# Optimization experiments

Hardware: AMD Instinct MI355X
Metric: run time of the kernel (lower is better)

The kernel has to match this reference:

```python
import jax, jax.numpy as jnp
import numpy as np
from math import sqrt

SCALE = sqrt(512.0)  # max(key_size, attn_hidden_size, query_size) with scaled=True

def setup_inputs() -> dict:
    key = jax.random.key(0)
    k1, k2, k3, k4, k5 = jax.random.split(key, 5)
    B, T, S, M, N, H = 8, 512, 512, 512, 512, 128
    return {
        "query": jax.random.normal(k1, (B, T, M), dtype=jnp.float32),
        "keys": jax.random.normal(k2, (B, S, N), dtype=jnp.float32),
        "W1": jax.random.normal(k3, (N, H), dtype=jnp.float32),
        "W2": jax.random.normal(k4, (M, H), dtype=jnp.float32),
        "v": jax.random.normal(k5, (H,), dtype=jnp.float32),
    }

def reference(query, keys, W1, W2, v):
    # Project query and keys into attention hidden space
    x1 = jnp.einsum('btm,mh->bth', query, W2)   # (B,T,H)
    x2 = jnp.einsum('bsn,nh->bsh', keys, W1)    # (B,S,H)
    # Broadcast merge (op='add'), tanh activation, v-weighted reduction over H
    merged = jnp.tanh(x1[:, :, None, :] + x2[:, None, :, :])  # (B,T,S,H)
    score = jnp.einsum('btsh,h->bts', merged, v)
    return score / SCALE
```

## Files before the change

kernel.cpp:

```cpp
#include <hip/hip_runtime.h>


constexpr float SCALE_IN  = 2.8853900817779268f;
constexpr float INV_SCALE = 0.04419417382415922f;

__global__ __launch_bounds__(512) void proj_kernel(
    const float* __restrict__ q,  const float* __restrict__ w2,
    const float* __restrict__ kk, const float* __restrict__ w1,
    float* __restrict__ x1w, float* __restrict__ x2w) {
  int blk = blockIdx.x;
  const float* A; const float* W; float* O;
  if (blk < 128) { A = q;  W = w2; O = x1w; }
  else           { blk -= 128; A = kk; W = w1; O = x2w; }

  const int tid = threadIdx.x;
  const int h   = tid & 127;
  const int rg  = tid >> 7;
  const int rbase = __builtin_amdgcn_readfirstlane(blk * 32 + rg * 8);

  float acc[8];
#pragma unroll
  for (int r = 0; r < 8; ++r) acc[r] = 0.0f;

  for (int m = 0; m < 512; m += 4) {
    const float wa = W[(m + 0) * 128 + h];
    const float wb = W[(m + 1) * 128 + h];
    const float wc = W[(m + 2) * 128 + h];
    const float wd = W[(m + 3) * 128 + h];
#pragma unroll
    for (int r = 0; r < 8; ++r) {
      const float4 a = *(const float4*)(A + (rbase + r) * 512 + m);
      acc[r] = fmaf(a.x, wa, acc[r]);
      acc[r] = fmaf(a.y, wb, acc[r]);
      acc[r] = fmaf(a.z, wc, acc[r]);
      acc[r] = fmaf(a.w, wd, acc[r]);
    }
  }
#pragma unroll
  for (int r = 0; r < 8; ++r)
    O[(rbase + r) * 128 + h] = acc[r] * SCALE_IN;
}

__global__ __launch_bounds__(256) void score_kernel(
    const float* __restrict__ x1w, const float* __restrict__ x2w,
    const float* __restrict__ v, float* __restrict__ out) {
  __shared__ float x1l[128 * 64];
  __shared__ float x2l[128 * 64];
  __shared__ float vl[128];

  const int tid   = threadIdx.x;
  const int b     = blockIdx.x >> 6;
  const int tile  = blockIdx.x & 63;
  const int tbase = (tile >> 3) * 64;
  const int sbase = (tile & 7) * 64;

  const float4* x1g = (const float4*)(x1w + (b * 512 + tbase) * 128);
  const float4* x2g = (const float4*)(x2w + (b * 512 + sbase) * 128);

  if (tid < 32) ((float4*)vl)[tid] = ((const float4*)v)[tid];

  const int l  = tid & 63;
  const int wv = tid >> 6;
#pragma unroll
  for (int p = 0; p < 8; ++p) {
    const int row = (l & 31) + 32 * (p & 1);
    const int c4  = (l >> 5) + 2 * wv + 8 * (p >> 1);
    const float4 a = x1g[row * 32 + c4];
    x1l[(4 * c4 + 0) * 64 + row] = a.x;
    x1l[(4 * c4 + 1) * 64 + row] = a.y;
    x1l[(4 * c4 + 2) * 64 + row] = a.z;
    x1l[(4 * c4 + 3) * 64 + row] = a.w;
    const float4 c = x2g[row * 32 + c4];
    x2l[(4 * c4 + 0) * 64 + row] = c.x;
    x2l[(4 * c4 + 1) * 64 + row] = c.y;
    x2l[(4 * c4 + 2) * 64 + row] = c.z;
    x2l[(4 * c4 + 3) * 64 + row] = c.w;
  }
  __syncthreads();

  const int sg = tid & 15;
  const int tg = tid >> 4;

  float racc[16];
#pragma unroll
  for (int i = 0; i < 16; ++i) racc[i] = 0.0f;
  float sv = 0.0f;

#pragma unroll 4
  for (int h = 0; h < 128; ++h) {
    const float4 tf = *(const float4*)(x1l + h * 64 + 4 * tg);
    const float4 sf = *(const float4*)(x2l + h * 64 + 4 * sg);
    const float vh = vl[h];
    sv += vh;
    const float ts[4] = {tf.x, tf.y, tf.z, tf.w};
    const float ss[4] = {sf.x, sf.y, sf.z, sf.w};
#pragma unroll
    for (int i = 0; i < 4; ++i) {
#pragma unroll
      for (int j = 0; j < 4; ++j) {
        const float e = __builtin_amdgcn_exp2f(ts[i] + ss[j]);
        const float r = __builtin_amdgcn_rcpf(e + 1.0f);
        racc[i * 4 + j] = fmaf(vh, r, racc[i * 4 + j]);
      }
    }
  }

  const float c1 = sv * INV_SCALE;
  const float c2 = -2.0f * INV_SCALE;
#pragma unroll
  for (int i = 0; i < 4; ++i) {
    const int t = tbase + 4 * tg + i;
    float4 o;
    o.x = fmaf(racc[i * 4 + 0], c2, c1);
    o.y = fmaf(racc[i * 4 + 1], c2, c1);
    o.z = fmaf(racc[i * 4 + 2], c2, c1);
    o.w = fmaf(racc[i * 4 + 3], c2, c1);
    *(float4*)(out + (size_t)(b * 512 + t) * 512 + sbase + 4 * sg) = o;
  }
}

extern "C" void kernel_launch(void* const* d_in, const int* in_sizes, int n_in,
                              void* d_out, int out_size, void* d_ws, size_t ws_size,
                              hipStream_t stream) {
  const float* query = (const float*)d_in[0];
  const float* keys  = (const float*)d_in[1];
  const float* W1    = (const float*)d_in[2];
  const float* W2    = (const float*)d_in[3];
  const float* v     = (const float*)d_in[4];
  float* out = (float*)d_out;

  float* x1w = (float*)d_ws;
  float* x2w = x1w + 8 * 512 * 128;

  hipLaunchKernelGGL(proj_kernel, dim3(256), dim3(512), 0, stream,
                     query, W2, keys, W1, x1w, x2w);
  hipLaunchKernelGGL(score_kernel, dim3(512), dim3(256), 0, stream,
                     x1w, x2w, v, out);
}
```

Before: 170.3 us.

## Precompute exp factors in projection and batch four reciprocals per rcp in score

The projection kernel now stores each exp2 value factored as an integer exponent plus an fp16 mantissa, packed into 32 bits. The score kernel rebuilds exp(x1+x2) with a multiply and ldexp instead of calling exp2 per element. It also sums four v-weighted reciprocals over a common denominator, so one rcp serves four h values. The projection GEMM moves to LDS tiling, and the score kernel runs 512 threads with fewer outputs per thread. This cuts transcendental work in the hot loop, but fp16 mantissas and the exponent clamp lose precision, and multiplying four terms into one denominator risks overflow.

```diff
diff --git a/kernel.cpp b/kernel.cpp
--- a/kernel.cpp
+++ b/kernel.cpp
@@ -1,4 +1,5 @@
 #include <hip/hip_runtime.h>
+#include <hip/hip_fp16.h>
 
 
 constexpr float SCALE_IN  = 2.8853900817779268f;
@@ -6,47 +7,81 @@
 
 __global__ __launch_bounds__(512) void proj_kernel(
     const float* __restrict__ q,  const float* __restrict__ w2,
-    const float* __restrict__ kk, const float* __restrict__ w1,
-    float* __restrict__ x1w, float* __restrict__ x2w) {
+    const float* __restrict__ ky, const float* __restrict__ w1,
+    unsigned int* __restrict__ x1w, unsigned int* __restrict__ x2w) {
+  __shared__ float As[32 * 64];
+  __shared__ float Ws[64 * 128];
+
   int blk = blockIdx.x;
-  const float* A; const float* W; float* O;
+  const float* A; const float* W; unsigned int* O;
   if (blk < 128) { A = q;  W = w2; O = x1w; }
-  else           { blk -= 128; A = kk; W = w1; O = x2w; }
-
+  else           { blk -= 128; A = ky; W = w1; O = x2w; }
+  const int rbase = blk * 32;
   const int tid = threadIdx.x;
-  const int h   = tid & 127;
-  const int rg  = tid >> 7;
-  const int rbase = __builtin_amdgcn_readfirstlane(blk * 32 + rg * 8);
-
-  float acc[8];
-#pragma unroll
-  for (int r = 0; r < 8; ++r) acc[r] = 0.0f;
-
-  for (int m = 0; m < 512; m += 4) {
-    const float wa = W[(m + 0) * 128 + h];
-    const float wb = W[(m + 1) * 128 + h];
-    const float wc = W[(m + 2) * 128 + h];
-    const float wd = W[(m + 3) * 128 + h];
-#pragma unroll
-    for (int r = 0; r < 8; ++r) {
-      const float4 a = *(const float4*)(A + (rbase + r) * 512 + m);
-      acc[r] = fmaf(a.x, wa, acc[r]);
-      acc[r] = fmaf(a.y, wb, acc[r]);
-      acc[r] = fmaf(a.z, wc, acc[r]);
-      acc[r] = fmaf(a.w, wd, acc[r]);
-    }
-  }
-#pragma unroll
-  for (int r = 0; r < 8; ++r)
-    O[(rbase + r) * 128 + h] = acc[r] * SCALE_IN;
+
+  const int rq = tid >> 5;
+  const int hq = tid & 31;
+
+  float acc[2][4];
+#pragma unroll
+  for (int r = 0; r < 2; ++r)
+#pragma unroll
+    for (int c = 0; c < 4; ++c) acc[r][c] = 0.0f;
+
+  for (int kb = 0; kb < 512; kb += 64) {
+    {
+      const int arow = tid >> 4;
+      const int kq4  = (tid & 15) * 4;
+      *(float4*)(As + arow * 64 + kq4) =
+          *(const float4*)(A + (size_t)(rbase + arow) * 512 + kb + kq4);
+      const int wrow = tid >> 5;
+      const int hq4  = (tid & 31) * 4;
+#pragma unroll
+      for (int p = 0; p < 4; ++p)
+        *(float4*)(Ws + (wrow + 16 * p) * 128 + hq4) =
+            *(const float4*)(W + (size_t)(kb + wrow + 16 * p) * 128 + hq4);
+    }
+    __syncthreads();
+#pragma unroll 4
+    for (int k4 = 0; k4 < 64; k4 += 4) {
+      float a[2][4], w[4][4];
+      *(float4*)a[0] = *(const float4*)(As + (2 * rq + 0) * 64 + k4);
+      *(float4*)a[1] = *(const float4*)(As + (2 * rq + 1) * 64 + k4);
+#pragma unroll
+      for (int kk = 0; kk < 4; ++kk)
+        *(float4*)w[kk] = *(const float4*)(Ws + (k4 + kk) * 128 + 4 * hq);
+#pragma unroll
+      for (int kk = 0; kk < 4; ++kk)
+#pragma unroll
+        for (int r = 0; r < 2; ++r)
+#pragma unroll
+          for (int c = 0; c < 4; ++c)
+            acc[r][c] = fmaf(a[r][kk], w[kk][c], acc[r][c]);
+    }
+    __syncthreads();
+  }
+
+#pragma unroll
+  for (int r = 0; r < 2; ++r) {
+    unsigned int pk[4];
+#pragma unroll
+    for (int c = 0; c < 4; ++c) {
+      const float z  = acc[r][c] * SCALE_IN;
+      const float kf = rintf(z);
+      const int   ki = (int)kf;
+      const float em = __builtin_amdgcn_exp2f(z - kf);
+      const __half hh = __float2half_rn(em);
+      pk[c] = ((unsigned int)ki << 16) | (unsigned int)__half_as_ushort(hh);
+    }
+    *(uint4*)(O + (size_t)(rbase + 2 * rq + r) * 128 + 4 * hq) = *(uint4*)pk;
+  }
 }
 
-__global__ __launch_bounds__(256) void score_kernel(
-    const float* __restrict__ x1w, const float* __restrict__ x2w,
+__global__ __launch_bounds__(512) void score_kernel(
+    const unsigned int* __restrict__ x1w, const unsigned int* __restrict__ x2w,
     const float* __restrict__ v, float* __restrict__ out) {
-  __shared__ float x1l[128 * 64];
-  __shared__ float x2l[128 * 64];
-  __shared__ float vl[128];
+  __shared__ unsigned int x1l[128 * 64];
+  __shared__ unsigned int x2l[128 * 64];
 
   const int tid   = threadIdx.x;
   const int b     = blockIdx.x >> 6;
@@ -54,23 +89,21 @@
   const int tbase = (tile >> 3) * 64;
   const int sbase = (tile & 7) * 64;
 
-  const float4* x1g = (const float4*)(x1w + (b * 512 + tbase) * 128);
-  const float4* x2g = (const float4*)(x2w + (b * 512 + sbase) * 128);
-
-  if (tid < 32) ((float4*)vl)[tid] = ((const float4*)v)[tid];
+  const uint4* x1g = (const uint4*)(x1w + (b * 512 + tbase) * 128);
+  const uint4* x2g = (const uint4*)(x2w + (b * 512 + sbase) * 128);
 
   const int l  = tid & 63;
-  const int wv = tid >> 6;
-#pragma unroll
-  for (int p = 0; p < 8; ++p) {
+  const int wq = tid >> 6;
+#pragma unroll
+  for (int p = 0; p < 4; ++p) {
     const int row = (l & 31) + 32 * (p & 1);
-    const int c4  = (l >> 5) + 2 * wv + 8 * (p >> 1);
-    const float4 a = x1g[row * 32 + c4];
+    const int c4  = (l >> 5) + 2 * wq + 16 * (p >> 1);
+    const uint4 a = x1g[row * 32 + c4];
     x1l[(4 * c4 + 0) * 64 + row] = a.x;
     x1l[(4 * c4 + 1) * 64 + row] = a.y;
     x1l[(4 * c4 + 2) * 64 + row] = a.z;
     x1l[(4 * c4 + 3) * 64 + row] = a.w;
-    const float4 c = x2g[row * 32 + c4];
+    const uint4 c = x2g[row * 32 + c4];
     x2l[(4 * c4 + 0) * 64 + row] = c.x;
     x2l[(4 * c4 + 1) * 64 + row] = c.y;
     x2l[(4 * c4 + 2) * 64 + row] = c.z;
@@ -81,26 +114,57 @@
   const int sg = tid & 15;
   const int tg = tid >> 4;
 
-  float racc[16];
-#pragma unroll
-  for (int i = 0; i < 16; ++i) racc[i] = 0.0f;
+  float racc[2][4];
+#pragma unroll
+  for (int i = 0; i < 2; ++i)
+#pragma unroll
+    for (int j = 0; j < 4; ++j) racc[i][j] = 0.0f;
   float sv = 0.0f;
 
-#pragma unroll 4
-  for (int h = 0; h < 128; ++h) {
-    const float4 tf = *(const float4*)(x1l + h * 64 + 4 * tg);
-    const float4 sf = *(const float4*)(x2l + h * 64 + 4 * sg);
-    const float vh = vl[h];
-    sv += vh;
-    const float ts[4] = {tf.x, tf.y, tf.z, tf.w};
-    const float ss[4] = {sf.x, sf.y, sf.z, sf.w};
-#pragma unroll
-    for (int i = 0; i < 4; ++i) {
+  for (int hg = 0; hg < 32; ++hg) {
+    const int h0 = hg * 4;
+    const float4 vq = *(const float4*)(v + h0);
+    sv += (vq.x + vq.y) + (vq.z + vq.w);
+
+    float emt[2][4]; int kt[2][4];
+    float ems[4][4]; int ks[4][4];
+#pragma unroll
+    for (int qq = 0; qq < 4; ++qq) {
+      const uint2 tp = *(const uint2*)(x1l + (h0 + qq) * 64 + 2 * tg);
+      emt[0][qq] = __half2float(__ushort_as_half((unsigned short)tp.x));
+      kt [0][qq] = ((int)tp.x) >> 16;
+      emt[1][qq] = __half2float(__ushort_as_half((unsigned short)tp.y));
+      kt [1][qq] = ((int)tp.y) >> 16;
+      const uint4 sp = *(const uint4*)(x2l + (h0 + qq) * 64 + 4 * sg);
+      ems[0][qq] = __half2float(__ushort_as_half((unsigned short)sp.x));
+      ks [0][qq] = ((int)sp.x) >> 16;
+      ems[1][qq] = __half2float(__ushort_as_half((unsigned short)sp.y));
+      ks [1][qq] = ((int)sp.y) >> 16;
+      ems[2][qq] = __half2float(__ushort_as_half((unsigned short)sp.z));
+      ks [2][qq] = ((int)sp.z) >> 16;
+      ems[3][qq] = __half2float(__ushort_as_half((unsigned short)sp.w));
+      ks [3][qq] = ((int)sp.w) >> 16;
+    }
+
+#pragma unroll
+    for (int i = 0; i < 2; ++i) {
 #pragma unroll
       for (int j = 0; j < 4; ++j) {
-        const float e = __builtin_amdgcn_exp2f(ts[i] + ss[j]);
-        const float r = __builtin_amdgcn_rcpf(e + 1.0f);
-        racc[i * 4 + j] = fmaf(vh, r, racc[i * 4 + j]);
+        float e[4];
+#pragma unroll
+        for (int qq = 0; qq < 4; ++qq) {
+          int kk = kt[i][qq] + ks[j][qq];
+          kk = min(kk, 30);
+          e[qq] = ldexpf(emt[i][qq] * ems[j][qq], kk);
+        }
+        const float a0 = e[0] + 1.0f, a1 = e[1] + 1.0f;
+        const float a2 = e[2] + 1.0f, a3 = e[3] + 1.0f;
+        const float p12 = a0 * a1, p34 = a2 * a3;
+        float u1 = vq.x * a1; u1 = fmaf(vq.y, a0, u1);
+        float u2 = vq.z * a3; u2 = fmaf(vq.w, a2, u2);
+        float num = u1 * p34; num = fmaf(u2, p12, num);
+        const float den = p12 * p34;
+        racc[i][j] = fmaf(num, __builtin_amdgcn_rcpf(den), racc[i][j]);
       }
     }
   }
@@ -108,13 +172,13 @@
   const float c1 = sv * INV_SCALE;
   const float c2 = -2.0f * INV_SCALE;
 #pragma unroll
-  for (int i = 0; i < 4; ++i) {
-    const int t = tbase + 4 * tg + i;
+  for (int i = 0; i < 2; ++i) {
+    const int t = tbase + 2 * tg + i;
     float4 o;
-    o.x = fmaf(racc[i * 4 + 0], c2, c1);
-    o.y = fmaf(racc[i * 4 + 1], c2, c1);
-    o.z = fmaf(racc[i * 4 + 2], c2, c1);
-    o.w = fmaf(racc[i * 4 + 3], c2, c1);
+    o.x = fmaf(racc[i][0], c2, c1);
+    o.y = fmaf(racc[i][1], c2, c1);
+    o.z = fmaf(racc[i][2], c2, c1);
+    o.w = fmaf(racc[i][3], c2, c1);
     *(float4*)(out + (size_t)(b * 512 + t) * 512 + sbase + 4 * sg) = o;
   }
 }
@@ -129,11 +193,11 @@
   const float* v     = (const float*)d_in[4];
   float* out = (float*)d_out;
 
-  float* x1w = (float*)d_ws;
-  float* x2w = x1w + 8 * 512 * 128;
+  unsigned int* x1w = (unsigned int*)d_ws;
+  unsigned int* x2w = x1w + 8 * 512 * 128;
 
   hipLaunchKernelGGL(proj_kernel, dim3(256), dim3(512), 0, stream,
                      query, W2, keys, W1, x1w, x2w);
-  hipLaunchKernelGGL(score_kernel, dim3(512), dim3(256), 0, stream,
+  hipLaunchKernelGGL(score_kernel, dim3(512), dim3(512), 0, stream,
                      x1w, x2w, v, out);
 }
```

Measured after the change: 145.7 us. 1.17x faster.
